# Kernel optimization log

Measured on AMD Instinct MI355X. Metric: run time of the kernel, lower is better.

Reference implementation:

```python
import jax, jax.numpy as jnp
import numpy as np

# Dims: batch B, channels C, spatial HxW; modes: weight spatial (32, 17) ('count' mode)
B, C, H, W = 8, 128, 128, 128
M_ROWS, M_COLS = 32, 17          # weight spatial size = [n_modes[0], n_modes[1]//2 + 1]
L_TOP = 17                       # n_modes[0]//2 + 1  -> rows [:17]
R_BOT = 15                       # n_modes[0] - L_TOP -> rows [-15:]


def setup_inputs() -> dict:
    key = jax.random.key(0)
    k1, k2, k3 = jax.random.split(key, 3)
    scale = C ** (-2)  # matches torch: scale * rand(..., cfloat) -> re/im ~ U[0, scale)
    X = jax.random.normal(k1, (B, C, H, W), dtype=jnp.float32)
    linear_re = scale * jax.random.uniform(k2, (C, C, M_ROWS, M_COLS), dtype=jnp.float32)
    linear_im = scale * jax.random.uniform(k3, (C, C, M_ROWS, M_COLS), dtype=jnp.float32)
    return {"X": X, "linear_re": linear_re, "linear_im": linear_im}


def _block(w_eff, xf):
    # w_eff: (C, C, m0, m1) complex, xf: (B, C, m0, m1) complex -> (B, C, m0, m1)
    return jnp.einsum('ctxy,btxy->bcxy', w_eff, xf)


def reference(X, linear_re, linear_im):
    Wc = linear_re + 1j * linear_im                       # (C, C, 32, 17) complex64
    # skew-Hermitian weight: linear - conj(linear).transpose(1, 0)
    W_eff = Wc - jnp.conj(jnp.swapaxes(Wc, 0, 1))
    Xf = jnp.fft.rfftn(X, axes=(-2, -1), norm='forward')  # (B, C, H, W//2+1) complex
    Y = jnp.zeros(Xf.shape, dtype=jnp.complex64)
    # corner block 1: low positive row frequencies
    Y = Y.at[:, :, :L_TOP, :M_COLS].set(
        _block(W_eff[:, :, :L_TOP, :], Xf[:, :, :L_TOP, :M_COLS]))
    # corner block 2: negative row frequencies
    Y = Y.at[:, :, -R_BOT:, :M_COLS].set(
        _block(W_eff[:, :, -R_BOT:, :], Xf[:, :, -R_BOT:, :M_COLS]))
    out = jnp.fft.irfftn(Y, s=(H, W), axes=(-2, -1), norm='forward')
    return out.astype(X.dtype)
```

## Files before the change

### kernel.cpp

```cpp
#include <hip/hip_runtime.h>
#include <math.h>

#define PI_F 3.14159265358979323846f

constexpr int NM = 544;

constexpr size_t OFF_F1T = 0;
constexpr size_t OFF_F2  = 17408;
constexpr size_t OFF_G   = 37888;
constexpr size_t OFF_CT  = 70656;
constexpr size_t OFF_XF  = 88064;
constexpr size_t OFF_YS  = 4544512;
constexpr size_t OFF_YP  = 9000960;

__global__ __launch_bounds__(256) void k_tab(float* __restrict__ F1T, float* __restrict__ F2,
                                             float2* __restrict__ G, float2* __restrict__ CT) {
  const int t0 = blockIdx.x * 256 + threadIdx.x;
  const int N = gridDim.x * 256;
  const float inv = 1.0f / 16384.0f;
  for (int i = t0; i < 17 * 128; i += N) {
    int r = i >> 7, x = i & 127;
    float s, c; sincosf(-2.f * PI_F * (float)((x * r) & 127) / 128.f, &s, &c);
    F1T[2 * i] = c * inv; F1T[2 * i + 1] = s * inv;
  }
  for (int i = t0; i < 128 * 20; i += N) {
    int y = i / 20, k = i - 20 * y;
    if (k >= 17) { F2[y * 40 + 2 * k] = 0.f; F2[y * 40 + 2 * k + 1] = 0.f; }
    else {
      float s, c; sincosf(-2.f * PI_F * (float)((y * k) & 127) / 128.f, &s, &c);
      F2[y * 40 + 2 * k] = c; F2[y * 40 + 2 * k + 1] = s;
    }
  }
  for (int i = t0; i < 32 * 128; i += N) {
    int r = i >> 7, x = i & 127;
    int f = (r < 17) ? r : r + 96;
    float s, c; sincosf(2.f * PI_F * (float)((f * x) & 127) / 128.f, &s, &c);
    G[i] = make_float2(c, s);
  }
  for (int i = t0; i < 17 * 128; i += N) {
    int k = i >> 7;
    float w = k ? 2.f : 1.f;
    float s, c; sincosf(2.f * PI_F * (float)((k * (i & 127)) & 127) / 128.f, &s, &c);
    CT[i] = make_float2(w * c, w * s);
  }
}

__global__ __launch_bounds__(256) void k_fwd(const float* __restrict__ X,
                                             const float* __restrict__ F1T,
                                             const float* __restrict__ F2G,
                                             float2* __restrict__ Xf) {
  __shared__ float tmpL[128 * 38];
  __shared__ float f2s[128 * 40];
  const int tid = threadIdx.x;
  const int bt = blockIdx.x;

  {
    const float4* src = (const float4*)F2G;
    float4* dst = (float4*)f2s;
    for (int i = tid; i < 1280; i += 256) dst[i] = src[i];
  }

  const int wid = __builtin_amdgcn_readfirstlane(tid >> 6);
  const int lane = tid & 63;
  const bool w0 = (wid == 0);
  const int r0 = wid * 4;

  for (int yh = 0; yh < 2; ++yh) {
    const int y = yh * 64 + lane;
    float2 acc[5];
#pragma unroll
    for (int i = 0; i < 5; ++i) acc[i] = make_float2(0.f, 0.f);
    const float* xp = X + (size_t)bt * 16384 + y;
    for (int xc = 0; xc < 32; ++xc) {
      const float* xq = xp + xc * 512;
      float v0 = xq[0], v1 = xq[128], v2 = xq[256], v3 = xq[384];
#pragma unroll
      for (int i = 0; i < 4; ++i) {
        const float* t = F1T + ((r0 + i) << 8) + (xc << 3);
        acc[i].x = fmaf(v0, t[0], acc[i].x); acc[i].y = fmaf(v0, t[1], acc[i].y);
        acc[i].x = fmaf(v1, t[2], acc[i].x); acc[i].y = fmaf(v1, t[3], acc[i].y);
        acc[i].x = fmaf(v2, t[4], acc[i].x); acc[i].y = fmaf(v2, t[5], acc[i].y);
        acc[i].x = fmaf(v3, t[6], acc[i].x); acc[i].y = fmaf(v3, t[7], acc[i].y);
      }
      if (w0) {
        const float* t = F1T + (16 << 8) + (xc << 3);
        acc[4].x = fmaf(v0, t[0], acc[4].x); acc[4].y = fmaf(v0, t[1], acc[4].y);
        acc[4].x = fmaf(v1, t[2], acc[4].x); acc[4].y = fmaf(v1, t[3], acc[4].y);
        acc[4].x = fmaf(v2, t[4], acc[4].x); acc[4].y = fmaf(v2, t[5], acc[4].y);
        acc[4].x = fmaf(v3, t[6], acc[4].x); acc[4].y = fmaf(v3, t[7], acc[4].y);
      }
    }
#pragma unroll
    for (int i = 0; i < 4; ++i) {
      tmpL[y * 38 + 2 * (r0 + i)]     = acc[i].x;
      tmpL[y * 38 + 2 * (r0 + i) + 1] = acc[i].y;
    }
    if (w0) { tmpL[y * 38 + 32] = acc[4].x; tmpL[y * 38 + 33] = acc[4].y; }
  }
  __syncthreads();

  const int r = lane & 31;
  const int yh = lane >> 5;
  const int r2 = (r < 17) ? r : 32 - r;
  const float sgn = (r < 17) ? 1.f : -1.f;
  const int ky0 = wid * 4;
  float2 a2[5];
#pragma unroll
  for (int i = 0; i < 5; ++i) a2[i] = make_float2(0.f, 0.f);
  const float* f2p = f2s + yh * 40 + 2 * ky0;
  const float* tp  = tmpL + yh * 38 + 2 * r2;
  for (int yl = 0; yl < 64; ++yl) {
    float2 tv = *(const float2*)tp;
    float tx = tv.x, ts = tv.y * sgn;
    float4 c01 = *(const float4*)(f2p);
    float4 c23 = *(const float4*)(f2p + 4);
    a2[0].x = fmaf(tx, c01.x, fmaf(-ts, c01.y, a2[0].x));
    a2[0].y = fmaf(tx, c01.y, fmaf( ts, c01.x, a2[0].y));
    a2[1].x = fmaf(tx, c01.z, fmaf(-ts, c01.w, a2[1].x));
    a2[1].y = fmaf(tx, c01.w, fmaf( ts, c01.z, a2[1].y));
    a2[2].x = fmaf(tx, c23.x, fmaf(-ts, c23.y, a2[2].x));
    a2[2].y = fmaf(tx, c23.y, fmaf( ts, c23.x, a2[2].y));
    a2[3].x = fmaf(tx, c23.z, fmaf(-ts, c23.w, a2[3].x));
    a2[3].y = fmaf(tx, c23.w, fmaf( ts, c23.z, a2[3].y));
    if (w0) {
      float2 c4 = *(const float2*)(f2p + 32);
      a2[4].x = fmaf(tx, c4.x, fmaf(-ts, c4.y, a2[4].x));
      a2[4].y = fmaf(tx, c4.y, fmaf( ts, c4.x, a2[4].y));
    }
    f2p += 80; tp += 76;
  }
#pragma unroll
  for (int i = 0; i < 5; ++i) {
    a2[i].x += __shfl_xor(a2[i].x, 32);
    a2[i].y += __shfl_xor(a2[i].y, 32);
  }
  if (lane < 32) {
    float2* xo = Xf + (size_t)bt * NM + r * 17 + ky0;
#pragma unroll
    for (int i = 0; i < 4; ++i) xo[i] = a2[i];
    if (w0) xo[16] = a2[4];
  }
}

__global__ __launch_bounds__(576) void k_mix(const float* __restrict__ Wre,
                                             const float* __restrict__ Wim,
                                             const float2* __restrict__ Xf,
                                             float2* __restrict__ Yp) {
  const int m = threadIdx.x;
  if (m >= NM) return;
  const int c = blockIdx.x & 127;
  const int q = blockIdx.x >> 7;
  const int chunk = q & 3;
  const int b0 = (q >> 2) * 4;
  float2 acc[4];
#pragma unroll
  for (int b = 0; b < 4; ++b) acc[b] = make_float2(0.f, 0.f);
  const int t0 = chunk * 32;
#pragma unroll 2
  for (int tt = 0; tt < 32; ++tt) {
    const int t = t0 + tt;
    float wr = Wre[(size_t)(c * 128 + t) * NM + m] - Wre[(size_t)(t * 128 + c) * NM + m];
    float wi = Wim[(size_t)(c * 128 + t) * NM + m] + Wim[(size_t)(t * 128 + c) * NM + m];
#pragma unroll
    for (int b = 0; b < 4; ++b) {
      float2 xv = Xf[(size_t)((b0 + b) * 128 + t) * NM + m];
      acc[b].x = fmaf(wr, xv.x, fmaf(-wi, xv.y, acc[b].x));
      acc[b].y = fmaf(wr, xv.y, fmaf(wi, xv.x, acc[b].y));
    }
  }
#pragma unroll
  for (int b = 0; b < 4; ++b)
    Yp[(size_t)chunk * 1024 * NM + (size_t)((b0 + b) * 128 + c) * NM + m] = acc[b];
}

__global__ __launch_bounds__(256) void k_red(const float2* __restrict__ Yp,
                                             float2* __restrict__ Ys) {
  int i = blockIdx.x * 256 + threadIdx.x;
  if (i >= 1024 * NM) return;
  int bc = i / NM, m = i - bc * NM;
  int r = m / 17, ky = m - r * 17;
  float2 s = make_float2(0.f, 0.f);
#pragma unroll
  for (int ch = 0; ch < 4; ++ch) {
    float2 v = Yp[(size_t)ch * 1024 * NM + i];
    s.x += v.x; s.y += v.y;
  }
  Ys[(size_t)bc * NM + ky * 32 + r] = s;
}

__global__ __launch_bounds__(256) void k_invB(const float* __restrict__ Ys,
                                              const float2* __restrict__ G,
                                              float2* __restrict__ Z) {
  const int tid = threadIdx.x;
  const int lane = tid & 63;
  const int xh = __builtin_amdgcn_readfirstlane((tid >> 6) & 1);
  const int p  = __builtin_amdgcn_readfirstlane(tid >> 7);
  const int x = xh * 64 + lane;
  const int bc = blockIdx.x;
  float2 g[32];
#pragma unroll
  for (int r = 0; r < 32; ++r) g[r] = G[r * 128 + x];
  const float* yb = Ys + (size_t)bc * (NM * 2);
  float2* zb = Z + (size_t)bc * (17 * 128) + x;
#pragma unroll
  for (int i = 0; i < 8; ++i) {
    const int ky = 2 * i + p;
    const float* yk = yb + ky * 64;
    float zr = 0.f, zi = 0.f;
#pragma unroll
    for (int r = 0; r < 32; ++r) {
      float ar = yk[2 * r], ai = yk[2 * r + 1];
      zr = fmaf(ar, g[r].x, fmaf(-ai, g[r].y, zr));
      zi = fmaf(ar, g[r].y, fmaf(ai, g[r].x, zi));
    }
    zb[ky * 128] = make_float2(zr, zi);
  }
  if (p == 0) {
    const float* yk = yb + 16 * 64;
    float zr = 0.f, zi = 0.f;
#pragma unroll
    for (int r = 0; r < 32; ++r) {
      float ar = yk[2 * r], ai = yk[2 * r + 1];
      zr = fmaf(ar, g[r].x, fmaf(-ai, g[r].y, zr));
      zi = fmaf(ar, g[r].y, fmaf(ai, g[r].x, zi));
    }
    zb[16 * 128] = make_float2(zr, zi);
  }
}

__global__ __launch_bounds__(256) void k_invC(const float* __restrict__ Z,
                                              const float2* __restrict__ CT,
                                              float* __restrict__ out) {
  const int tid = threadIdx.x;
  const int yy = tid & 127;
  const int xh = __builtin_amdgcn_readfirstlane(tid >> 7);
  const int bc = blockIdx.x;
  float2 ct[17];
#pragma unroll
  for (int k = 0; k < 17; ++k) ct[k] = CT[k * 128 + yy];
  const float* zb = Z + (size_t)bc * (17 * 128 * 2);
  float* op = out + (size_t)bc * 16384;
#pragma unroll 2
  for (int xi = 0; xi < 64; ++xi) {
    int x = xh * 64 + xi;
    const float* zp = zb + 2 * x;
    float s = 0.f;
#pragma unroll
    for (int k = 0; k < 17; ++k) {
      float zr = zp[k * 256], zi = zp[k * 256 + 1];
      s = fmaf(zr, ct[k].x, fmaf(-zi, ct[k].y, s));
    }
    op[x * 128 + yy] = s;
  }
}

extern "C" void kernel_launch(void* const* d_in, const int* in_sizes, int n_in,
                              void* d_out, int out_size, void* d_ws, size_t ws_size,
                              hipStream_t stream) {
  const float* X   = (const float*)d_in[0];
  const float* Wre = (const float*)d_in[1];
  const float* Wim = (const float*)d_in[2];
  float* out = (float*)d_out;

  char* ws = (char*)d_ws;
  float*  F1T = (float*)(ws + OFF_F1T);
  float*  F2  = (float*)(ws + OFF_F2);
  float2* G   = (float2*)(ws + OFF_G);
  float2* CT  = (float2*)(ws + OFF_CT);
  float2* Xf  = (float2*)(ws + OFF_XF);
  float2* Ys  = (float2*)(ws + OFF_YS);
  float2* Yp  = (float2*)(ws + OFF_YP);
  float2* Z   = Yp;

  k_tab <<<32, 256, 0, stream>>>(F1T, F2, G, CT);
  k_fwd <<<1024, 256, 0, stream>>>(X, F1T, F2, Xf);
  k_mix <<<1024, 576, 0, stream>>>(Wre, Wim, Xf, Yp);
  k_red <<<2176, 256, 0, stream>>>(Yp, Ys);
  k_invB<<<1024, 256, 0, stream>>>((const float*)Ys, G, Z);
  k_invC<<<1024, 256, 0, stream>>>((const float*)Z, CT, out);
}
```

Measured before the change: 336.5 us.

## Process all 8 batches per mixing block with software-prefetched loads and XCD swizzle

The channel-mixing kernel now gives each block all 8 batch items instead of 4. Each skew-Hermitian weight pair is therefore read once rather than twice, and the grid is halved to 512 blocks. The inner loop double-buffers the next iteration's weight and spectrum loads in registers to hide memory latency. Block indices are remapped so neighbouring work groups land on the same XCD. In exchange each thread holds more registers, and the grid is smaller, which may reduce occupancy.

New measurement: 336.0 us. About the same (-0.2%).

```diff
diff --git a/kernel.cpp b/kernel.cpp
--- a/kernel.cpp
+++ b/kernel.cpp
@@ -148,29 +148,65 @@
                                              float2* __restrict__ Yp) {
   const int m = threadIdx.x;
   if (m >= NM) return;
-  const int c = blockIdx.x & 127;
-  const int q = blockIdx.x >> 7;
-  const int chunk = q & 3;
-  const int b0 = (q >> 2) * 4;
-  float2 acc[4];
-#pragma unroll
-  for (int b = 0; b < 4; ++b) acc[b] = make_float2(0.f, 0.f);
-  const int t0 = chunk * 32;
+  const int bid = blockIdx.x;
+  const int wg = ((bid & 7) << 6) | (bid >> 3);
+  const int q = wg >> 7;
+  const int c = wg & 127;
+  const int t0 = q * 32;
+
+  const float* wre_ct = Wre + (size_t)(c * 128 + t0) * NM + m;
+  const float* wre_tc = Wre + (size_t)(t0 * 128 + c) * NM + m;
+  const float* wim_ct = Wim + (size_t)(c * 128 + t0) * NM + m;
+  const float* wim_tc = Wim + (size_t)(t0 * 128 + c) * NM + m;
+  const float2* xp = Xf + (size_t)t0 * NM + m;
+
+  float2 acc[8];
+#pragma unroll
+  for (int b = 0; b < 8; ++b) acc[b] = make_float2(0.f, 0.f);
+
+  float a_re = wre_ct[0];
+  float b_re = wre_tc[0];
+  float a_im = wim_ct[0];
+  float b_im = wim_tc[0];
+  float2 xv[8];
+#pragma unroll
+  for (int b = 0; b < 8; ++b) xv[b] = xp[b * 128 * NM];
+
 #pragma unroll 2
-  for (int tt = 0; tt < 32; ++tt) {
-    const int t = t0 + tt;
-    float wr = Wre[(size_t)(c * 128 + t) * NM + m] - Wre[(size_t)(t * 128 + c) * NM + m];
-    float wi = Wim[(size_t)(c * 128 + t) * NM + m] + Wim[(size_t)(t * 128 + c) * NM + m];
-#pragma unroll
-    for (int b = 0; b < 4; ++b) {
-      float2 xv = Xf[(size_t)((b0 + b) * 128 + t) * NM + m];
-      acc[b].x = fmaf(wr, xv.x, fmaf(-wi, xv.y, acc[b].x));
-      acc[b].y = fmaf(wr, xv.y, fmaf(wi, xv.x, acc[b].y));
-    }
-  }
-#pragma unroll
-  for (int b = 0; b < 4; ++b)
-    Yp[(size_t)chunk * 1024 * NM + (size_t)((b0 + b) * 128 + c) * NM + m] = acc[b];
+  for (int tt = 0; tt < 31; ++tt) {
+    float n_are = wre_ct[(tt + 1) * NM];
+    float n_bre = wre_tc[(tt + 1) * 128 * NM];
+    float n_aim = wim_ct[(tt + 1) * NM];
+    float n_bim = wim_tc[(tt + 1) * 128 * NM];
+    float2 nxv[8];
+#pragma unroll
+    for (int b = 0; b < 8; ++b) nxv[b] = xp[(tt + 1) * NM + b * 128 * NM];
+
+    float wr = a_re - b_re;
+    float wi = a_im + b_im;
+#pragma unroll
+    for (int b = 0; b < 8; ++b) {
+      acc[b].x = fmaf(wr, xv[b].x, fmaf(-wi, xv[b].y, acc[b].x));
+      acc[b].y = fmaf(wr, xv[b].y, fmaf( wi, xv[b].x, acc[b].y));
+    }
+
+    a_re = n_are; b_re = n_bre; a_im = n_aim; b_im = n_bim;
+#pragma unroll
+    for (int b = 0; b < 8; ++b) xv[b] = nxv[b];
+  }
+  {
+    float wr = a_re - b_re;
+    float wi = a_im + b_im;
+#pragma unroll
+    for (int b = 0; b < 8; ++b) {
+      acc[b].x = fmaf(wr, xv[b].x, fmaf(-wi, xv[b].y, acc[b].x));
+      acc[b].y = fmaf(wr, xv[b].y, fmaf( wi, xv[b].x, acc[b].y));
+    }
+  }
+
+#pragma unroll
+  for (int b = 0; b < 8; ++b)
+    Yp[(size_t)q * 1024 * NM + (size_t)(b * 128 + c) * NM + m] = acc[b];
 }
 
 __global__ __launch_bounds__(256) void k_red(const float2* __restrict__ Yp,
@@ -274,7 +310,7 @@
 
   k_tab <<<32, 256, 0, stream>>>(F1T, F2, G, CT);
   k_fwd <<<1024, 256, 0, stream>>>(X, F1T, F2, Xf);
-  k_mix <<<1024, 576, 0, stream>>>(Wre, Wim, Xf, Yp);
+  k_mix <<<512, 576, 0, stream>>>(Wre, Wim, Xf, Yp);
   k_red <<<2176, 256, 0, stream>>>(Yp, Ys);
   k_invB<<<1024, 256, 0, stream>>>((const float*)Ys, G, Z);
   k_invC<<<1024, 256, 0, stream>>>((const float*)Z, CT, out);
```

## Double-buffer mode-mixing operands in LDS via direct global-to-LDS loads

Applied to the files above, without the earlier changes.

Rewrites the spectral mixing kernel so each block computes two output channels, sharing the staged Xf slices between them. Weights and Xf slices for each input channel are staged into a double-buffered LDS area with global_load_lds DMA, with per-wave vmcnt waits and barriers so loading the next step overlaps compute on the current one. A bid swizzle remaps blocks to improve locality, and the grid is halved. This targets the memory-bound Xf and weight reads, at the cost of large LDS use (about 70KB per block), two barriers per step, and a fragile hand-counted waitcnt scheme.

Result: no change. 339.4 us (+0.9%).

```diff
diff --git a/kernel.cpp b/kernel.cpp
--- a/kernel.cpp
+++ b/kernel.cpp
@@ -142,35 +142,138 @@
   }
 }
 
-__global__ __launch_bounds__(576) void k_mix(const float* __restrict__ Wre,
-                                             const float* __restrict__ Wim,
-                                             const float2* __restrict__ Xf,
-                                             float2* __restrict__ Yp) {
-  const int m = threadIdx.x;
-  if (m >= NM) return;
-  const int c = blockIdx.x & 127;
-  const int q = blockIdx.x >> 7;
-  const int chunk = q & 3;
-  const int b0 = (q >> 2) * 4;
-  float2 acc[4];
-#pragma unroll
-  for (int b = 0; b < 4; ++b) acc[b] = make_float2(0.f, 0.f);
-  const int t0 = chunk * 32;
-#pragma unroll 2
+
+__device__ __forceinline__ void ldsdma16(const float* g, float* l) {
+  __builtin_amdgcn_global_load_lds(
+      (const __attribute__((address_space(1))) void*)g,
+      (__attribute__((address_space(3))) void*)l, 16, 0, 0);
+}
+__device__ __forceinline__ void ldsdma4(const float* g, float* l) {
+  __builtin_amdgcn_global_load_lds(
+      (const __attribute__((address_space(1))) void*)g,
+      (__attribute__((address_space(3))) void*)l, 4, 0, 0);
+}
+
+__device__ __forceinline__ void stage544(const float* src, float* dst, int lane) {
+  ldsdma16(src + 4 * lane,        dst);
+  ldsdma16(src + 256 + 4 * lane,  dst + 256);
+  ldsdma4 (src + 480 + lane,      dst + 480);
+}
+__device__ __forceinline__ void stage1088(const float* src, float* dst, int lane) {
+#pragma unroll
+  for (int k = 0; k < 4; ++k) ldsdma16(src + 256 * k + 4 * lane, dst + 256 * k);
+  ldsdma4(src + 1024 + lane, dst + 1024);
+}
+
+__device__ __forceinline__ void stage_mix(int wid, int lane, float* buf,
+                                          const float* Wre, const float* Wim,
+                                          const float* Xff, int c0, int b0, int ta) {
+  switch (wid) {
+    case 0:
+      stage544(Wre + (size_t)(c0 * 128 + ta) * NM,       buf,        lane);
+      stage544(Wre + (size_t)((c0 + 1) * 128 + ta) * NM, buf + 544,  lane);
+      break;
+    case 1:
+      stage544(Wim + (size_t)(c0 * 128 + ta) * NM,       buf + 1088, lane);
+      stage544(Wim + (size_t)((c0 + 1) * 128 + ta) * NM, buf + 1632, lane);
+      break;
+    case 2:
+      stage1088(Wre + ((size_t)ta * 128 + c0) * NM,      buf + 2176, lane);
+      break;
+    case 3:
+      stage1088(Wim + ((size_t)ta * 128 + c0) * NM,      buf + 3264, lane);
+      break;
+    case 4:
+      stage1088(Xff + (size_t)((b0 + 0) * 128 + ta) * NM * 2, buf + 4352 + 0 * 1088, lane);
+      break;
+    case 5:
+      stage1088(Xff + (size_t)((b0 + 1) * 128 + ta) * NM * 2, buf + 4352 + 1 * 1088, lane);
+      break;
+    case 6:
+      stage1088(Xff + (size_t)((b0 + 2) * 128 + ta) * NM * 2, buf + 4352 + 2 * 1088, lane);
+      break;
+    case 7:
+      stage1088(Xff + (size_t)((b0 + 3) * 128 + ta) * NM * 2, buf + 4352 + 3 * 1088, lane);
+      break;
+    default: break;
+  }
+}
+
+#define WAITV(N) asm volatile("s_waitcnt vmcnt(" #N ")" ::: "memory")
+
+__global__ __launch_bounds__(576, 2) void k_mix(const float* __restrict__ Wre,
+                                                const float* __restrict__ Wim,
+                                                const float2* __restrict__ Xf,
+                                                float2* __restrict__ Yp) {
+  __shared__ float lds[2][8704];
+  const int tid = threadIdx.x;
+  const int lane = tid & 63;
+  const int wid = __builtin_amdgcn_readfirstlane(tid >> 6);
+  const int m = tid;
+  const int bid = blockIdx.x;
+  const int wg = ((bid & 7) << 6) | (bid >> 3);
+  const int bh = wg >> 8;
+  const int q  = (wg >> 6) & 3;
+  const int c0 = (wg & 63) << 1;
+  const int b0 = bh * 4;
+  const int t0 = q * 32;
+  const float* Xff = (const float*)Xf;
+
+  float2 acc0[4], acc1[4];
+#pragma unroll
+  for (int b = 0; b < 4; ++b) {
+    acc0[b] = make_float2(0.f, 0.f);
+    acc1[b] = make_float2(0.f, 0.f);
+  }
+
+  stage_mix(wid, lane, lds[0], Wre, Wim, Xff, c0, b0, t0 + 0);
+  stage_mix(wid, lane, lds[1], Wre, Wim, Xff, c0, b0, t0 + 1);
+
   for (int tt = 0; tt < 32; ++tt) {
-    const int t = t0 + tt;
-    float wr = Wre[(size_t)(c * 128 + t) * NM + m] - Wre[(size_t)(t * 128 + c) * NM + m];
-    float wi = Wim[(size_t)(c * 128 + t) * NM + m] + Wim[(size_t)(t * 128 + c) * NM + m];
+    if (tt < 31) {
+      if (wid < 2)      WAITV(6);
+      else if (wid < 8) WAITV(5);
+      else              WAITV(0);
+    } else {
+      WAITV(0);
+    }
+    __builtin_amdgcn_sched_barrier(0);
+    __builtin_amdgcn_s_barrier();
+    __builtin_amdgcn_sched_barrier(0);
+
+    const float* B = &lds[tt & 1][0];
+    if (m < NM) {
+      float ar0 = B[m],        ar1 = B[544 + m];
+      float ai0 = B[1088 + m], ai1 = B[1632 + m];
+      float br0 = B[2176 + m], br1 = B[2176 + 544 + m];
+      float bi0 = B[3264 + m], bi1 = B[3264 + 544 + m];
+      float wr0 = ar0 - br0, wi0 = ai0 + bi0;
+      float wr1 = ar1 - br1, wi1 = ai1 + bi1;
+#pragma unroll
+      for (int b = 0; b < 4; ++b) {
+        float2 xv = *(const float2*)(B + 4352 + b * 1088 + 2 * m);
+        acc0[b].x = fmaf(wr0, xv.x, fmaf(-wi0, xv.y, acc0[b].x));
+        acc0[b].y = fmaf(wr0, xv.y, fmaf( wi0, xv.x, acc0[b].y));
+        acc1[b].x = fmaf(wr1, xv.x, fmaf(-wi1, xv.y, acc1[b].x));
+        acc1[b].y = fmaf(wr1, xv.y, fmaf( wi1, xv.x, acc1[b].y));
+      }
+    }
+    __builtin_amdgcn_sched_barrier(0);
+    __builtin_amdgcn_s_barrier();
+    __builtin_amdgcn_sched_barrier(0);
+
+    if (tt + 2 < 32)
+      stage_mix(wid, lane, lds[tt & 1], Wre, Wim, Xff, c0, b0, t0 + tt + 2);
+  }
+
+  if (m < NM) {
+    float2* yb = Yp + (size_t)q * 1024 * NM + m;
 #pragma unroll
     for (int b = 0; b < 4; ++b) {
-      float2 xv = Xf[(size_t)((b0 + b) * 128 + t) * NM + m];
-      acc[b].x = fmaf(wr, xv.x, fmaf(-wi, xv.y, acc[b].x));
-      acc[b].y = fmaf(wr, xv.y, fmaf(wi, xv.x, acc[b].y));
-    }
-  }
-#pragma unroll
-  for (int b = 0; b < 4; ++b)
-    Yp[(size_t)chunk * 1024 * NM + (size_t)((b0 + b) * 128 + c) * NM + m] = acc[b];
+      yb[(size_t)((b0 + b) * 128 + c0)     * NM] = acc0[b];
+      yb[(size_t)((b0 + b) * 128 + c0 + 1) * NM] = acc1[b];
+    }
+  }
 }
 
 __global__ __launch_bounds__(256) void k_red(const float2* __restrict__ Yp,
@@ -274,7 +377,7 @@
 
   k_tab <<<32, 256, 0, stream>>>(F1T, F2, G, CT);
   k_fwd <<<1024, 256, 0, stream>>>(X, F1T, F2, Xf);
-  k_mix <<<1024, 576, 0, stream>>>(Wre, Wim, Xf, Yp);
+  k_mix <<<512, 576, 0, stream>>>(Wre, Wim, Xf, Yp);
   k_red <<<2176, 256, 0, stream>>>(Yp, Ys);
   k_invB<<<1024, 256, 0, stream>>>((const float*)Ys, G, Z);
   k_invC<<<1024, 256, 0, stream>>>((const float*)Z, CT, out);
```

## Restructure channel-mix kernel with float4 mode vectorization and full-batch weight reuse

Applied to the files above, without the earlier changes.

Each thread in the mode-mixing kernel now handles 4 consecutive modes with float4 loads, and each block covers all 8 batches (two per thread) instead of 4. This halves the number of times the weight tensors, including the transposed reads, are fetched. Block indices are swizzled to spread the work, and the grid is halved. The cost is more registers per thread and fewer blocks in flight.

Result: no change. 339.2 us (+0.8%).

```diff
diff --git a/kernel.cpp b/kernel.cpp
--- a/kernel.cpp
+++ b/kernel.cpp
@@ -142,35 +142,75 @@
   }
 }
 
-__global__ __launch_bounds__(576) void k_mix(const float* __restrict__ Wre,
-                                             const float* __restrict__ Wim,
-                                             const float2* __restrict__ Xf,
-                                             float2* __restrict__ Yp) {
-  const int m = threadIdx.x;
-  if (m >= NM) return;
-  const int c = blockIdx.x & 127;
-  const int q = blockIdx.x >> 7;
-  const int chunk = q & 3;
-  const int b0 = (q >> 2) * 4;
-  float2 acc[4];
-#pragma unroll
-  for (int b = 0; b < 4; ++b) acc[b] = make_float2(0.f, 0.f);
-  const int t0 = chunk * 32;
-#pragma unroll 2
+__global__ __launch_bounds__(576, 5) void k_mix(const float* __restrict__ Wre,
+                                                const float* __restrict__ Wim,
+                                                const float2* __restrict__ Xf,
+                                                float2* __restrict__ Yp) {
+  const int tid = threadIdx.x;
+  if (tid >= 544) return;
+  const int bid = blockIdx.x;
+  const int wg = ((bid & 7) << 6) | (bid >> 3);
+  const int q = wg >> 7;
+  const int c = wg & 127;
+  const int t0 = q * 32;
+  const int bq = tid / 136;
+  const int mq = tid - bq * 136;
+  const int m4 = mq << 2;
+
+  const float* Xff = (const float*)Xf;
+  const float* wct_re = Wre + (size_t)(c * 128 + t0) * NM + m4;
+  const float* wct_im = Wim + (size_t)(c * 128 + t0) * NM + m4;
+  const float* wtc_re = Wre + ((size_t)t0 * 128 + c) * NM + m4;
+  const float* wtc_im = Wim + ((size_t)t0 * 128 + c) * NM + m4;
+  const float* x0 = Xff + ((size_t)((bq    ) * 128 + t0) * NM + m4) * 2;
+  const float* x1 = Xff + ((size_t)((bq + 4) * 128 + t0) * NM + m4) * 2;
+
+  float2 a0[4], a1[4];
+#pragma unroll
+  for (int j = 0; j < 4; ++j) {
+    a0[j] = make_float2(0.f, 0.f);
+    a1[j] = make_float2(0.f, 0.f);
+  }
+
   for (int tt = 0; tt < 32; ++tt) {
-    const int t = t0 + tt;
-    float wr = Wre[(size_t)(c * 128 + t) * NM + m] - Wre[(size_t)(t * 128 + c) * NM + m];
-    float wi = Wim[(size_t)(c * 128 + t) * NM + m] + Wim[(size_t)(t * 128 + c) * NM + m];
-#pragma unroll
-    for (int b = 0; b < 4; ++b) {
-      float2 xv = Xf[(size_t)((b0 + b) * 128 + t) * NM + m];
-      acc[b].x = fmaf(wr, xv.x, fmaf(-wi, xv.y, acc[b].x));
-      acc[b].y = fmaf(wr, xv.y, fmaf(wi, xv.x, acc[b].y));
-    }
-  }
-#pragma unroll
-  for (int b = 0; b < 4; ++b)
-    Yp[(size_t)chunk * 1024 * NM + (size_t)((b0 + b) * 128 + c) * NM + m] = acc[b];
+    float4 cre = *(const float4*)(wct_re + (size_t)tt * NM);
+    float4 cim = *(const float4*)(wct_im + (size_t)tt * NM);
+    float4 tre = *(const float4*)(wtc_re + (size_t)tt * 128 * NM);
+    float4 tim = *(const float4*)(wtc_im + (size_t)tt * 128 * NM);
+    float4 xa0 = *(const float4*)(x0 + (size_t)tt * NM * 2);
+    float4 xb0 = *(const float4*)(x0 + (size_t)tt * NM * 2 + 4);
+    float4 xa1 = *(const float4*)(x1 + (size_t)tt * NM * 2);
+    float4 xb1 = *(const float4*)(x1 + (size_t)tt * NM * 2 + 4);
+
+    float wr, wi;
+    wr = cre.x - tre.x; wi = cim.x + tim.x;
+    a0[0].x = fmaf(wr, xa0.x, fmaf(-wi, xa0.y, a0[0].x));
+    a0[0].y = fmaf(wr, xa0.y, fmaf( wi, xa0.x, a0[0].y));
+    a1[0].x = fmaf(wr, xa1.x, fmaf(-wi, xa1.y, a1[0].x));
+    a1[0].y = fmaf(wr, xa1.y, fmaf( wi, xa1.x, a1[0].y));
+    wr = cre.y - tre.y; wi = cim.y + tim.y;
+    a0[1].x = fmaf(wr, xa0.z, fmaf(-wi, xa0.w, a0[1].x));
+    a0[1].y = fmaf(wr, xa0.w, fmaf( wi, xa0.z, a0[1].y));
+    a1[1].x = fmaf(wr, xa1.z, fmaf(-wi, xa1.w, a1[1].x));
+    a1[1].y = fmaf(wr, xa1.w, fmaf( wi, xa1.z, a1[1].y));
+    wr = cre.z - tre.z; wi = cim.z + tim.z;
+    a0[2].x = fmaf(wr, xb0.x, fmaf(-wi, xb0.y, a0[2].x));
+    a0[2].y = fmaf(wr, xb0.y, fmaf( wi, xb0.x, a0[2].y));
+    a1[2].x = fmaf(wr, xb1.x, fmaf(-wi, xb1.y, a1[2].x));
+    a1[2].y = fmaf(wr, xb1.y, fmaf( wi, xb1.x, a1[2].y));
+    wr = cre.w - tre.w; wi = cim.w + tim.w;
+    a0[3].x = fmaf(wr, xb0.z, fmaf(-wi, xb0.w, a0[3].x));
+    a0[3].y = fmaf(wr, xb0.w, fmaf( wi, xb0.z, a0[3].y));
+    a1[3].x = fmaf(wr, xb1.z, fmaf(-wi, xb1.w, a1[3].x));
+    a1[3].y = fmaf(wr, xb1.w, fmaf( wi, xb1.z, a1[3].y));
+  }
+
+  float* yp0 = (float*)(Yp + (size_t)q * 1024 * NM + (size_t)(bq * 128 + c) * NM + m4);
+  float* yp1 = (float*)(Yp + (size_t)q * 1024 * NM + (size_t)((bq + 4) * 128 + c) * NM + m4);
+  *(float4*)(yp0)     = make_float4(a0[0].x, a0[0].y, a0[1].x, a0[1].y);
+  *(float4*)(yp0 + 4) = make_float4(a0[2].x, a0[2].y, a0[3].x, a0[3].y);
+  *(float4*)(yp1)     = make_float4(a1[0].x, a1[0].y, a1[1].x, a1[1].y);
+  *(float4*)(yp1 + 4) = make_float4(a1[2].x, a1[2].y, a1[3].x, a1[3].y);
 }
 
 __global__ __launch_bounds__(256) void k_red(const float2* __restrict__ Yp,
@@ -274,7 +314,7 @@
 
   k_tab <<<32, 256, 0, stream>>>(F1T, F2, G, CT);
   k_fwd <<<1024, 256, 0, stream>>>(X, F1T, F2, Xf);
-  k_mix <<<1024, 576, 0, stream>>>(Wre, Wim, Xf, Yp);
+  k_mix <<<512, 576, 0, stream>>>(Wre, Wim, Xf, Yp);
   k_red <<<2176, 256, 0, stream>>>(Yp, Ys);
   k_invB<<<1024, 256, 0, stream>>>((const float*)Ys, G, Z);
   k_invC<<<1024, 256, 0, stream>>>((const float*)Z, CT, out);
```
